# Optimization experiments

Measured on AMD Instinct MI355X. Metric: run time of the kernel, lower is better.

The kernel has to match this reference:

```python
import jax, jax.numpy as jnp
import numpy as np
from jax import lax

BN_EPS = 1e-3
SLOPE = 0.1
CLUSTER_TEMP = 30.0
K = 16
FEAT = 4096  # 8*8*64


def conv_bn_lrelu(x, w, b, g, beta, m, v):
    # Conv2d stride 2, padding 1 (NCHW / OIHW), then eval-mode BatchNorm, then LeakyReLU.
    y = lax.conv_general_dilated(x, w, window_strides=(2, 2), padding=((1, 1), (1, 1)),
                                 dimension_numbers=("NCHW", "OIHW", "NCHW"))
    y = y + b[None, :, None, None]
    scale = g / jnp.sqrt(v + BN_EPS)
    y = y * scale[None, :, None, None] + (beta - m * scale)[None, :, None, None]
    return jnp.where(y > 0, y, SLOPE * y)


def soft_kmeans(data, mu, num_iter, ct):
    # Row L2-normalize (equivalent to diag(1/||x||) @ data)
    data = data / jnp.linalg.norm(data, axis=1, keepdims=True)
    for _ in range(num_iter):
        dist = data @ mu.T                      # [N, K]
        r = jax.nn.softmax(ct * dist, axis=1)   # [N, K]
        mu = (r.T @ data) / r.sum(axis=0)[:, None]  # [K, F]
    dist = data @ mu.T
    r = jax.nn.softmax(ct * dist, axis=1)
    return mu, r, dist


def setup_inputs() -> dict:
    key = jax.random.key(0)
    ks = jax.random.split(key, 12)
    d = {}
    d["x"] = jax.random.normal(ks[0], (256, 3, 64, 64), dtype=jnp.float32)
    # conv1: 3 -> 128
    d["conv1_w"] = jax.random.normal(ks[1], (128, 3, 3, 3), dtype=jnp.float32) * 0.05
    d["conv1_b"] = jnp.zeros((128,), jnp.float32)
    d["bn1_g"] = jnp.ones((128,), jnp.float32)
    d["bn1_b"] = jnp.zeros((128,), jnp.float32)
    d["bn1_m"] = jax.random.normal(ks[2], (128,), dtype=jnp.float32) * 0.1
    d["bn1_v"] = jax.random.uniform(ks[3], (128,), minval=0.5, maxval=1.5, dtype=jnp.float32)
    # conv2: 128 -> 256
    d["conv2_w"] = jax.random.normal(ks[4], (256, 128, 3, 3), dtype=jnp.float32) * 0.02
    d["conv2_b"] = jnp.zeros((256,), jnp.float32)
    d["bn2_g"] = jnp.ones((256,), jnp.float32)
    d["bn2_b"] = jnp.zeros((256,), jnp.float32)
    d["bn2_m"] = jax.random.normal(ks[5], (256,), dtype=jnp.float32) * 0.1
    d["bn2_v"] = jax.random.uniform(ks[6], (256,), minval=0.5, maxval=1.5, dtype=jnp.float32)
    # conv3: 256 -> 64
    d["conv3_w"] = jax.random.normal(ks[7], (64, 256, 3, 3), dtype=jnp.float32) * 0.02
    d["conv3_b"] = jnp.zeros((64,), jnp.float32)
    d["bn3_g"] = jnp.ones((64,), jnp.float32)
    d["bn3_b"] = jnp.zeros((64,), jnp.float32)
    d["bn3_m"] = jax.random.normal(ks[8], (64,), dtype=jnp.float32) * 0.1
    d["bn3_v"] = jax.random.uniform(ks[9], (64,), minval=0.5, maxval=1.5, dtype=jnp.float32)
    # initial cluster centers, torch.rand(K, F)
    d["mu0"] = jax.random.uniform(ks[10], (K, FEAT), dtype=jnp.float32)
    d["num_iter"] = 10
    return d


def reference(x, conv1_w, conv1_b, bn1_g, bn1_b, bn1_m, bn1_v,
              conv2_w, conv2_b, bn2_g, bn2_b, bn2_m, bn2_v,
              conv3_w, conv3_b, bn3_g, bn3_b, bn3_m, bn3_v,
              mu0, num_iter):
    h = conv_bn_lrelu(x, conv1_w, conv1_b, bn1_g, bn1_b, bn1_m, bn1_v)   # [B,128,32,32]
    h = conv_bn_lrelu(h, conv2_w, conv2_b, bn2_g, bn2_b, bn2_m, bn2_v)   # [B,256,16,16]
    h = conv_bn_lrelu(h, conv3_w, conv3_b, bn3_g, bn3_b, bn3_m, bn3_v)   # [B,64,8,8]
    embeds = h.reshape(-1, FEAT)                                          # [B, 4096]
    mu_init, _, _ = soft_kmeans(embeds, mu0, num_iter, CLUSTER_TEMP)
    _, r, _ = soft_kmeans(embeds, lax.stop_gradient(mu_init), 1, CLUSTER_TEMP)
    return r
```

## Files before the change

kernel.cpp:

```cpp
#include <hip/hip_runtime.h>
#include <stdint.h>
#include <stddef.h>

typedef unsigned short u16;
typedef __attribute__((ext_vector_type(8))) short short8;
typedef __attribute__((ext_vector_type(4))) float f32x4;
typedef __attribute__((ext_vector_type(4))) int int4v;

__device__ __forceinline__ float bf2f(u16 u) {
    unsigned x = ((unsigned)u) << 16;
    return __uint_as_float(x);
}
__device__ __forceinline__ u16 f2bf(float f) {
    unsigned x = __float_as_uint(f);
    unsigned r = (x + 0x7fffu + ((x >> 16) & 1u)) >> 16;
    return (u16)r;
}
__device__ __forceinline__ float ldin(const void* p, size_t i, int isbf) {
    return isbf ? bf2f(((const u16*)p)[i]) : ((const float*)p)[i];
}
__device__ __forceinline__ int detect_bf(const void* v1) {
    const u16* ub = (const u16*)v1;
    int ok = 1;
#pragma unroll
    for (int i = 0; i < 16; i++) {
        float f = bf2f(ub[i]);
        if (!(f >= 0.4f && f <= 1.6f)) ok = 0;
    }
    return ok;
}
__device__ __forceinline__ int sw(int r, int c8) {
    return r * 32 + (((c8) ^ (r & 3)) << 3);
}

struct PrepArgs {
    const void *w1, *w2, *w3;
    u16 *W1p, *W2p, *W3p;
    const void *b1, *g1, *be1, *m1, *v1;
    const void *b2, *g2, *be2, *m2, *v2;
    const void *b3, *g3, *be3, *m3, *v3;
    float *es1, *esh1, *es2, *esh2, *es3, *esh3;
};
__device__ __forceinline__ void packw_body(const void* src, u16* dst, int CI, int Kp,
                                           int total, int blk, int t, int isbf) {
    int p = blk * 256 + t;
    if (p >= total) return;
    int co = p / Kp, k = p - co * Kp;
    int tap = k / CI, ci = k - tap * CI;
    u16 v = 0;
    if (tap < 9) {
        size_t si = (size_t)(co * CI + ci) * 9 + tap;
        v = isbf ? ((const u16*)src)[si] : f2bf(((const float*)src)[si]);
    }
    dst[p] = v;
}
__global__ __launch_bounds__(256) void kprep_all(PrepArgs A) {
    int b = blockIdx.x, t = threadIdx.x;
    int isbf = detect_bf(A.v1);
    if (b < 1152) {
        packw_body(A.w2, A.W2p, 128, 1152, 256 * 1152, b, t, isbf);
    } else if (b < 1728) {
        packw_body(A.w3, A.W3p, 256, 2304, 64 * 2304, b - 1152, t, isbf);
    } else if (b < 1744) {
        packw_body(A.w1, A.W1p, 3, 32, 128 * 32, b - 1728, t, isbf);
    } else {
        int u = (b - 1744) * 256 + t;
        const void *bb, *g, *be, *m, *v;
        float *es, *esh;
        int c;
        if (u < 128)      { c = u;       bb=A.b1; g=A.g1; be=A.be1; m=A.m1; v=A.v1; es=A.es1; esh=A.esh1; }
        else if (u < 384) { c = u - 128; bb=A.b2; g=A.g2; be=A.be2; m=A.m2; v=A.v2; es=A.es2; esh=A.esh2; }
        else if (u < 448) { c = u - 384; bb=A.b3; g=A.g3; be=A.be3; m=A.m3; v=A.v3; es=A.es3; esh=A.esh3; }
        else return;
        float sc = ldin(g, c, isbf) / sqrtf(ldin(v, c, isbf) + 1e-3f);
        float sh = (ldin(bb, c, isbf) - ldin(m, c, isbf)) * sc + ldin(be, c, isbf);
        es[c] = sc;
        esh[c] = sh;
    }
}

__global__ void kfallback(u16* __restrict__ out) {
    int i = blockIdx.x * 256 + threadIdx.x;
    if (i < 4096) out[i] = f2bf(0.0625f);
}

__global__ __launch_bounds__(256) void im2col1(const void* __restrict__ x,
                                               u16* __restrict__ A1,
                                               const void* __restrict__ v1ref) {
    int n = blockIdx.x, t = threadIdx.x;
    int isbf = detect_bf(v1ref);
    __shared__ u16 xs[3 * 64 * 64];
    if (isbf) {
        const u16* xp = (const u16*)x + (size_t)n * 12288;
#pragma unroll
        for (int i = t * 8; i < 12288; i += 2048)
            *(int4v*)&xs[i] = *(const int4v*)&xp[i];
    } else {
        const float* xp = (const float*)x + (size_t)n * 12288;
#pragma unroll
        for (int i = t * 4; i < 12288; i += 1024) {
            float4 v = *(const float4*)&xp[i];
            xs[i] = f2bf(v.x); xs[i + 1] = f2bf(v.y);
            xs[i + 2] = f2bf(v.z); xs[i + 3] = f2bf(v.w);
        }
    }
    __syncthreads();
#pragma unroll
    for (int rr = 0; rr < 4; rr++) {
        int m = rr * 256 + t;
        int ox = m & 31, oy = m >> 5;
        alignas(16) u16 row[32];
#pragma unroll
        for (int k = 0; k < 32; k++) {
            u16 val = 0;
            if (k < 27) {
                int tap = k / 3, ci = k - 3 * tap;
                int ky = tap / 3, kx = tap - 3 * ky;
                int iy = 2 * oy - 1 + ky, ix = 2 * ox - 1 + kx;
                if ((unsigned)iy < 64u && (unsigned)ix < 64u)
                    val = xs[ci * 4096 + iy * 64 + ix];
            }
            row[k] = val;
        }
        int4v* dst = (int4v*)(A1 + ((size_t)n * 1024 + m) * 32);
        const int4v* srcv = (const int4v*)row;
#pragma unroll
        for (int q = 0; q < 4; q++) dst[q] = srcv[q];
    }
}

__global__ __launch_bounds__(256) void gemm_conv1(
    const u16* __restrict__ A1, const u16* __restrict__ W,
    const float* __restrict__ es, const float* __restrict__ esh,
    u16* __restrict__ OutB) {
    alignas(16) __shared__ u16 As[128 * 32];
    alignas(16) __shared__ u16 Bs[128 * 32];
    const int t = threadIdx.x;
    const int m0 = blockIdx.x * 128;
    const int lane = t & 63, w = t >> 6;
    const int wm = w & 1, wn = w >> 1;
    const int rA = t >> 2, c8 = t & 3, koff = c8 * 8;

#pragma unroll
    for (int j = 0; j < 2; j++) {
        int4v va = *(const int4v*)(A1 + (size_t)(m0 + j * 64 + rA) * 32 + koff);
        *(int4v*)&As[sw(j * 64 + rA, c8)] = va;
        int4v vb = *(const int4v*)(W + (size_t)(j * 64 + rA) * 32 + koff);
        *(int4v*)&Bs[sw(j * 64 + rA, c8)] = vb;
    }
    __syncthreads();
    const int qc = lane >> 4, fr = lane & 15;
    short8 af[4], bf[4];
#pragma unroll
    for (int i = 0; i < 4; i++) af[i] = *(const short8*)&As[sw(wm * 64 + i * 16 + fr, qc)];
#pragma unroll
    for (int j = 0; j < 4; j++) bf[j] = *(const short8*)&Bs[sw(wn * 64 + j * 16 + fr, qc)];
    f32x4 acc[4][4];
#pragma unroll
    for (int i = 0; i < 4; i++)
#pragma unroll
        for (int j = 0; j < 4; j++) {
#pragma unroll
            for (int q = 0; q < 4; q++) acc[i][j][q] = 0.f;
            acc[i][j] = __builtin_amdgcn_mfma_f32_16x16x32_bf16(af[i], bf[j], acc[i][j], 0, 0, 0);
        }
#pragma unroll
    for (int j = 0; j < 4; j++) {
        int c = wn * 64 + j * 16 + fr;
        float sc = es[c], sh = esh[c];
#pragma unroll
        for (int i = 0; i < 4; i++) {
#pragma unroll
            for (int rg = 0; rg < 4; rg++) {
                int m = m0 + wm * 64 + i * 16 + qc * 4 + rg;
                float v = acc[i][j][rg] * sc + sh;
                v = (v > 0.f) ? v : 0.1f * v;
                int ox = m & 31, oy = (m >> 5) & 31, n = m >> 10;
                OutB[((size_t)(n * 32 + oy) * 32 + ox) * 128 + c] = f2bf(v);
            }
        }
    }
}

__global__ __launch_bounds__(256) void gemm_conv2(
    const u16* __restrict__ Asrc, const u16* __restrict__ W,
    const float* __restrict__ es, const float* __restrict__ esh,
    u16* __restrict__ OutB) {
    constexpr int CIN = 128, KTOT = 1152, OHW = 16, LOG_OHW = 4, IH = 32;
    constexpr int CC = 4, AR = 2, BR = 2, SM = 4, SN = 4;

    alignas(16) __shared__ u16 As[128 * 32];
    alignas(16) __shared__ u16 Bs[128 * 32];

    const int t = threadIdx.x;
    const int lid = blockIdx.x;
    const int xcd = lid & 7, slot = lid >> 3;
    const int img = xcd * 32 + (slot >> 2);
    const int sub = slot & 3;
    const int m0 = img * 256 + (sub & 1) * 128;
    const int n0 = (sub >> 1) * 128;
    const int lane = t & 63, w = t >> 6;
    const int wm = w & 1, wn = w >> 1;
    const int rA = t >> 2, c8 = t & 3, koff = c8 * 8;
    const int fr = lane & 15, qc = lane >> 4;

    f32x4 acc[SM][SN];
#pragma unroll
    for (int i = 0; i < SM; i++)
#pragma unroll
        for (int j = 0; j < SN; j++)
#pragma unroll
            for (int q = 0; q < 4; q++) acc[i][j][q] = 0.0f;

    int aox[AR], aoy[AR], an_[AR];
#pragma unroll
    for (int j = 0; j < AR; j++) {
        int m = m0 + j * 64 + rA;
        aox[j] = m & (OHW - 1);
        aoy[j] = (m >> LOG_OHW) & (OHW - 1);
        an_[j] = m >> (2 * LOG_OHW);
    }
    auto mkoffs = [&](int j, int tap) -> int {
        int ky = tap / 3, kx = tap - 3 * ky;
        int iy = 2 * aoy[j] - 1 + ky, ix = 2 * aox[j] - 1 + kx;
        if ((unsigned)iy < (unsigned)IH && (unsigned)ix < (unsigned)IH)
            return ((an_[j] * IH + iy) * IH + ix) * CIN;
        return -0x40000000;
    };
    const u16* Wrow[BR];
#pragma unroll
    for (int j = 0; j < BR; j++)
        Wrow[j] = W + (size_t)(n0 + j * 64 + rA) * KTOT + koff;

    int offs_cur[AR], offs_nxt[AR];
#pragma unroll
    for (int j = 0; j < AR; j++) offs_cur[j] = mkoffs(j, 0);

    const int4v zerov = (int4v){0, 0, 0, 0};
    int4v bufA[2][AR], bufB[2][BR];
#pragma unroll
    for (int pp = 0; pp < 2; pp++) {
#pragma unroll
        for (int j = 0; j < AR; j++)
            bufA[pp][j] = (offs_cur[j] >= 0)
                              ? *(const int4v*)(Asrc + offs_cur[j] + pp * 32 + koff)
                              : zerov;
#pragma unroll
        for (int j = 0; j < BR; j++) bufB[pp][j] = *(const int4v*)(Wrow[j] + pp * 32);
    }

    int flat = 0;
    for (int tap = 0; tap < 9; tap++) {
#pragma unroll
        for (int j = 0; j < AR; j++)
            offs_nxt[j] = (tap < 8) ? mkoffs(j, tap + 1) : -0x40000000;
#pragma unroll
        for (int cc = 0; cc < CC; cc++, flat++) {
            const int pb_ = flat & 1;
#pragma unroll
            for (int j = 0; j < AR; j++) *(int4v*)&As[sw(j * 64 + rA, c8)] = bufA[pb_][j];
#pragma unroll
            for (int j = 0; j < BR; j++) *(int4v*)&Bs[sw(j * 64 + rA, c8)] = bufB[pb_][j];
            __syncthreads();
            {
                const int cc2 = cc + 2;
                const bool intap = (cc2 < CC);
                const int cci = intap ? cc2 : cc2 - CC;
                const int aoffbase = cci * 32 + koff;
#pragma unroll
                for (int j = 0; j < AR; j++) {
                    int o = intap ? offs_cur[j] : offs_nxt[j];
                    bufA[pb_][j] = (o >= 0) ? *(const int4v*)(Asrc + o + aoffbase) : zerov;
                }
                const bool wvalid = intap || (tap < 8);
                const int wk = (intap ? tap : tap + 1) * CIN + cci * 32;
#pragma unroll
                for (int j = 0; j < BR; j++)
                    bufB[pb_][j] = wvalid ? *(const int4v*)(Wrow[j] + wk) : zerov;
            }
            short8 af[SM], bf[SN];
#pragma unroll
            for (int i = 0; i < SM; i++)
                af[i] = *(const short8*)&As[sw(wm * 64 + i * 16 + fr, qc)];
#pragma unroll
            for (int j = 0; j < SN; j++)
                bf[j] = *(const short8*)&Bs[sw(wn * 64 + j * 16 + fr, qc)];
#pragma unroll
            for (int i = 0; i < SM; i++)
#pragma unroll
                for (int j = 0; j < SN; j++)
                    acc[i][j] = __builtin_amdgcn_mfma_f32_16x16x32_bf16(
                        af[i], bf[j], acc[i][j], 0, 0, 0);
            __syncthreads();
        }
#pragma unroll
        for (int j = 0; j < AR; j++) offs_cur[j] = offs_nxt[j];
    }

#pragma unroll
    for (int j = 0; j < SN; j++) {
        int c = n0 + wn * 64 + j * 16 + fr;
        float sc = es[c], sh = esh[c];
#pragma unroll
        for (int i = 0; i < SM; i++) {
#pragma unroll
            for (int rg = 0; rg < 4; rg++) {
                int row = wm * 64 + i * 16 + qc * 4 + rg;
                int m = m0 + row;
                float v = acc[i][j][rg] * sc + sh;
                v = (v > 0.f) ? v : 0.1f * v;
                int ox = m & (OHW - 1), oy = (m >> LOG_OHW) & (OHW - 1), n = m >> (2 * LOG_OHW);
                OutB[((size_t)(n * 16 + oy) * 16 + ox) * 256 + c] = f2bf(v);
            }
        }
    }
}

__global__ __launch_bounds__(256) void gemm_conv3f(
    const u16* __restrict__ Asrc, const u16* __restrict__ W,
    const float* __restrict__ es3, const float* __restrict__ esh3,
    float* __restrict__ dat, u16* __restrict__ datbf) {
    constexpr int CIN = 256, KTOT = 2304, IH = 16;
    constexpr int CC = 8, SM = 2, SN = 2;

    alignas(16) __shared__ u16 As[64 * 32];
    alignas(16) __shared__ u16 Bs[64 * 32];
    __shared__ float red[4];

    const int t = threadIdx.x;
    const int lid = blockIdx.x;
    const int xcd = lid & 7, slot = lid >> 3;
    const int img = xcd * 32 + slot;
    const int m0 = img * 64;
    const int lane = t & 63, w = t >> 6;
    const int wm = w & 1, wn = w >> 1;
    const int rA = t >> 2, c8 = t & 3, koff = c8 * 8;
    const int fr = lane & 15, qc = lane >> 4;

    f32x4 acc[SM][SN];
#pragma unroll
    for (int i = 0; i < SM; i++)
#pragma unroll
        for (int j = 0; j < SN; j++)
#pragma unroll
            for (int q = 0; q < 4; q++) acc[i][j][q] = 0.0f;

    const int aox = rA & 7, aoy = (rA >> 3) & 7;
    auto mkoffs = [&](int tap) -> int {
        int ky = tap / 3, kx = tap - 3 * ky;
        int iy = 2 * aoy - 1 + ky, ix = 2 * aox - 1 + kx;
        if ((unsigned)iy < (unsigned)IH && (unsigned)ix < (unsigned)IH)
            return ((img * IH + iy) * IH + ix) * CIN;
        return -0x40000000;
    };
    const u16* Wrow = W + (size_t)rA * KTOT + koff;

    int offs_cur = mkoffs(0), offs_nxt;
    const int4v zerov = (int4v){0, 0, 0, 0};
    int4v bufA[2], bufB[2];
#pragma unroll
    for (int pp = 0; pp < 2; pp++) {
        bufA[pp] = (offs_cur >= 0)
                       ? *(const int4v*)(Asrc + offs_cur + pp * 32 + koff)
                       : zerov;
        bufB[pp] = *(const int4v*)(Wrow + pp * 32);
    }

    int flat = 0;
    for (int tap = 0; tap < 9; tap++) {
        offs_nxt = (tap < 8) ? mkoffs(tap + 1) : -0x40000000;
#pragma unroll
        for (int cc = 0; cc < CC; cc++, flat++) {
            const int pb_ = flat & 1;
            *(int4v*)&As[sw(rA, c8)] = bufA[pb_];
            *(int4v*)&Bs[sw(rA, c8)] = bufB[pb_];
            __syncthreads();
            {
                const int cc2 = cc + 2;
                const bool intap = (cc2 < CC);
                const int cci = intap ? cc2 : cc2 - CC;
                int o = intap ? offs_cur : offs_nxt;
                bufA[pb_] = (o >= 0) ? *(const int4v*)(Asrc + o + cci * 32 + koff) : zerov;
                const bool wvalid = intap || (tap < 8);
                const int wk = (intap ? tap : tap + 1) * CIN + cci * 32;
                bufB[pb_] = wvalid ? *(const int4v*)(Wrow + wk) : zerov;
            }
            short8 af[SM], bf[SN];
#pragma unroll
            for (int i = 0; i < SM; i++)
                af[i] = *(const short8*)&As[sw(wm * 32 + i * 16 + fr, qc)];
#pragma unroll
            for (int j = 0; j < SN; j++)
                bf[j] = *(const short8*)&Bs[sw(wn * 32 + j * 16 + fr, qc)];
#pragma unroll
            for (int i = 0; i < SM; i++)
#pragma unroll
                for (int j = 0; j < SN; j++)
                    acc[i][j] = __builtin_amdgcn_mfma_f32_16x16x32_bf16(
                        af[i], bf[j], acc[i][j], 0, 0, 0);
            __syncthreads();
        }
        offs_cur = offs_nxt;
    }

    float vals[SM][SN][4];
    float ssq = 0.f;
#pragma unroll
    for (int j = 0; j < SN; j++) {
        int c = wn * 32 + j * 16 + fr;
        float sc = es3[c], sh = esh3[c];
#pragma unroll
        for (int i = 0; i < SM; i++) {
#pragma unroll
            for (int rg = 0; rg < 4; rg++) {
                float v = acc[i][j][rg] * sc + sh;
                v = (v > 0.f) ? v : 0.1f * v;
                vals[i][j][rg] = v;
                ssq += v * v;
            }
        }
    }
#pragma unroll
    for (int off = 32; off > 0; off >>= 1) ssq += __shfl_xor(ssq, off);
    if (lane == 0) red[w] = ssq;
    __syncthreads();
    float inv = 1.0f / sqrtf(red[0] + red[1] + red[2] + red[3]);
#pragma unroll
    for (int j = 0; j < SN; j++) {
        int c = wn * 32 + j * 16 + fr;
#pragma unroll
        for (int i = 0; i < SM; i++) {
#pragma unroll
            for (int rg = 0; rg < 4; rg++) {
                int row = wm * 32 + i * 16 + qc * 4 + rg;
                size_t idx = (size_t)img * 4096 + c * 64 + row;
                float v = vals[i][j][rg] * inv;
                dat[idx] = v;
                datbf[idx] = f2bf(v);
            }
        }
    }
}

__global__ __launch_bounds__(256) void kgr(const u16* __restrict__ dbf,
                                           const float* __restrict__ dat,
                                           const void* __restrict__ mu0,
                                           u16* __restrict__ Ghi,
                                           u16* __restrict__ Glo,
                                           float* __restrict__ rb0,
                                           const void* __restrict__ v1ref) {
    const int b = blockIdx.x, t = threadIdx.x;
    alignas(16) __shared__ u16 As[64 * 32];
    alignas(16) __shared__ u16 Bs[64 * 32];
    __shared__ float part[16][4];
    __shared__ float ds[16];

    if (b < 16) {
        const int m0 = (b & 3) * 64, n0 = (b >> 2) * 64;
        const int lane = t & 63, w = t >> 6;
        const int wm = w & 1, wn = w >> 1;
        const int rA = t >> 2, c8 = t & 3, koff = c8 * 8;

        f32x4 acc[2][2];
#pragma unroll
        for (int i = 0; i < 2; i++)
#pragma unroll
            for (int j = 0; j < 2; j++)
#pragma unroll
                for (int q = 0; q < 4; q++) acc[i][j][q] = 0.0f;

        int4v pa = *(const int4v*)(dbf + (size_t)(m0 + rA) * 4096 + koff);
        int4v pb = *(const int4v*)(dbf + (size_t)(n0 + rA) * 4096 + koff);
        for (int it = 0; it < 128; it++) {
            *(int4v*)&As[sw(rA, c8)] = pa;
            *(int4v*)&Bs[sw(rA, c8)] = pb;
            __syncthreads();
            if (it + 1 < 128) {
                int k = (it + 1) * 32 + koff;
                pa = *(const int4v*)(dbf + (size_t)(m0 + rA) * 4096 + k);
                pb = *(const int4v*)(dbf + (size_t)(n0 + rA) * 4096 + k);
            }
            const int qc = lane >> 4, fr = lane & 15;
            short8 af[2], bf[2];
#pragma unroll
            for (int i = 0; i < 2; i++) af[i] = *(const short8*)&As[sw(wm * 32 + i * 16 + fr, qc)];
#pragma unroll
            for (int j = 0; j < 2; j++) bf[j] = *(const short8*)&Bs[sw(wn * 32 + j * 16 + fr, qc)];
#pragma unroll
            for (int i = 0; i < 2; i++)
#pragma unroll
                for (int j = 0; j < 2; j++)
                    acc[i][j] = __builtin_amdgcn_mfma_f32_16x16x32_bf16(af[i], bf[j], acc[i][j], 0, 0, 0);
            if (it + 1 < 128) __syncthreads();
        }
#pragma unroll
        for (int j = 0; j < 2; j++) {
            int c = n0 + wn * 32 + j * 16 + (lane & 15);
#pragma unroll
            for (int i = 0; i < 2; i++)
#pragma unroll
                for (int rg = 0; rg < 4; rg++) {
                    int row = m0 + wm * 32 + i * 16 + (lane >> 4) * 4 + rg;
                    float v = acc[i][j][rg];
                    u16 hi = f2bf(v);
                    u16 lo = f2bf(v - bf2f(hi));
                    Ghi[(size_t)row * 256 + c] = hi;
                    Glo[(size_t)row * 256 + c] = lo;
                }
        }
    } else {
        const int n = b - 16;
        const int isbf = detect_bf(v1ref);
        const int lane = t & 63, wv = t >> 6;
        float d[16];
#pragma unroll
        for (int j = 0; j < 16; j++) d[j] = dat[(size_t)n * 4096 + j * 256 + t];
#pragma unroll
        for (int k = 0; k < 16; k++) {
            float a = 0.f;
            if (isbf) {
                const u16* mp = (const u16*)mu0 + (size_t)k * 4096;
#pragma unroll
                for (int j = 0; j < 16; j++) a = fmaf(d[j], bf2f(mp[j * 256 + t]), a);
            } else {
                const float* mp = (const float*)mu0 + (size_t)k * 4096;
#pragma unroll
                for (int j = 0; j < 16; j++) a = fmaf(d[j], mp[j * 256 + t], a);
            }
#pragma unroll
            for (int off = 32; off > 0; off >>= 1) a += __shfl_xor(a, off);
            if (lane == 0) part[k][wv] = a;
        }
        __syncthreads();
        if (t < 16) {
            float dk = part[t][0] + part[t][1] + part[t][2] + part[t][3];
            ds[t] = dk;
            __syncthreads();
            float mx = -1e30f;
#pragma unroll
            for (int j = 0; j < 16; j++) mx = fmaxf(mx, ds[j]);
            float sum = 0.f;
#pragma unroll
            for (int j = 0; j < 16; j++) sum += __expf(30.f * (ds[j] - mx));
            rb0[n * 16 + t] = __expf(30.f * (dk - mx)) / sum;
        }
    }
}

__global__ __launch_bounds__(1024) void kmiter(const u16* __restrict__ Ghi,
                                               const u16* __restrict__ Glo,
                                               const float* __restrict__ rb0,
                                               void* __restrict__ dout,
                                               const void* __restrict__ v1ref) {
    const int t = threadIdx.x;
    const int isbf = detect_bf(v1ref);
    const int lane = t & 63, w = t >> 6;
    const int i0 = w * 16;
    const int col = lane & 15;
    const int q = lane >> 4;

    __shared__ float rf[4096];
    __shared__ u16 rThi[16 * 264];
    __shared__ u16 rTlo[16 * 264];
    __shared__ float part[16][17];
    __shared__ float rs[16];

    for (int idx = t; idx < 4096; idx += 1024) {
        float v = rb0[idx];
        rf[idx] = v;
        u16 hi = f2bf(v);
        rThi[(idx & 15) * 264 + (idx >> 4)] = hi;
        rTlo[(idx & 15) * 264 + (idx >> 4)] = f2bf(v - bf2f(hi));
    }
    __syncthreads();

    const u16* Ahirow = Ghi + (size_t)(i0 + col) * 256 + q * 8;
    const u16* Alorow = Glo + (size_t)(i0 + col) * 256 + q * 8;
    for (int iter = 0; iter < 11; iter++) {
        f32x4 acc = {0.f, 0.f, 0.f, 0.f};
#pragma unroll
        for (int ks = 0; ks < 256; ks += 32) {
            short8 ah = *(const short8*)(Ahirow + ks);
            short8 al = *(const short8*)(Alorow + ks);
            short8 bh = *(const short8*)&rThi[col * 264 + ks + q * 8];
            short8 bl = *(const short8*)&rTlo[col * 264 + ks + q * 8];
            acc = __builtin_amdgcn_mfma_f32_16x16x32_bf16(ah, bh, acc, 0, 0, 0);
            acc = __builtin_amdgcn_mfma_f32_16x16x32_bf16(al, bh, acc, 0, 0, 0);
            acc = __builtin_amdgcn_mfma_f32_16x16x32_bf16(ah, bl, acc, 0, 0, 0);
        }
        if (t < 256) {
            int kk = t & 15, g = t >> 4;
            float psum = 0.f;
#pragma unroll
            for (int nn = 0; nn < 16; nn++) psum += rf[(g * 16 + nn) * 16 + kk];
            part[kk][g] = psum;
        }
        __syncthreads();
        if (t < 16) {
            float ssum = 0.f;
#pragma unroll
            for (int g = 0; g < 16; g++) ssum += part[t][g];
            rs[t] = ssum;
        }
        __syncthreads();
        float rsc = rs[col];
        float rv[4];
#pragma unroll
        for (int rg = 0; rg < 4; rg++) {
            float dk = acc[rg] / rsc;
            float mx = dk;
#pragma unroll
            for (int o = 1; o < 16; o <<= 1) mx = fmaxf(mx, __shfl_xor(mx, o));
            float e = __expf(30.f * (dk - mx));
            float ssum = e;
#pragma unroll
            for (int o = 1; o < 16; o <<= 1) ssum += __shfl_xor(ssum, o);
            rv[rg] = e / ssum;
        }
        if (iter < 10) {
            __syncthreads();
#pragma unroll
            for (int rg = 0; rg < 4; rg++) {
                int row = i0 + q * 4 + rg;
                float v = rv[rg];
                rf[row * 16 + col] = v;
                u16 hi = f2bf(v);
                rThi[col * 264 + row] = hi;
                rTlo[col * 264 + row] = f2bf(v - bf2f(hi));
            }
            __syncthreads();
        } else {
#pragma unroll
            for (int rg = 0; rg < 4; rg++) {
                int row = i0 + q * 4 + rg;
                if (isbf) ((u16*)dout)[row * 16 + col] = f2bf(rv[rg]);
                else ((float*)dout)[row * 16 + col] = rv[rg];
            }
        }
    }
}

extern "C" void kernel_launch(void* const* d_in, const int* in_sizes, int n_in,
                              void* d_out, int out_size, void* d_ws, size_t ws_size,
                              hipStream_t stream) {
    const void* x   = d_in[0];
    const void* w1  = d_in[1];
    const void* b1  = d_in[2];
    const void* g1  = d_in[3];
    const void* be1 = d_in[4];
    const void* m1  = d_in[5];
    const void* v1  = d_in[6];
    const void* w2  = d_in[7];
    const void* b2  = d_in[8];
    const void* g2  = d_in[9];
    const void* be2 = d_in[10];
    const void* m2  = d_in[11];
    const void* v2  = d_in[12];
    const void* w3  = d_in[13];
    const void* b3  = d_in[14];
    const void* g3  = d_in[15];
    const void* be3 = d_in[16];
    const void* m3  = d_in[17];
    const void* v3  = d_in[18];
    const void* mu0 = d_in[19];

    char* p = (char*)d_ws;
    size_t used = 0;
    auto alloc = [&](size_t bytes) -> char* {
        char* q = p;
        size_t rb = (bytes + 255) & ~(size_t)255;
        p += rb;
        used += rb;
        return q;
    };
    float* rb0 = (float*)alloc(4096 * 4);
    u16* Ghi = (u16*)alloc((size_t)65536 * 2);
    u16* Glo = (u16*)alloc((size_t)65536 * 2);
    u16* W1p = (u16*)alloc((size_t)128 * 32 * 2);
    u16* W2p = (u16*)alloc((size_t)256 * 1152 * 2);
    u16* W3p = (u16*)alloc((size_t)64 * 2304 * 2);
    float* es1 = (float*)alloc(128 * 4);
    float* esh1 = (float*)alloc(128 * 4);
    float* es2 = (float*)alloc(256 * 4);
    float* esh2 = (float*)alloc(256 * 4);
    float* es3 = (float*)alloc(64 * 4);
    float* esh3 = (float*)alloc(64 * 4);
    const size_t R1 = (size_t)256 * 32 * 32 * 128 * 2;
    const size_t R2 = (size_t)256 * 16 * 16 * 256 * 2;
    char* reg1 = alloc(R1);
    char* reg2 = alloc(R2);
    u16* h1 = (u16*)reg1;
    u16* A1 = (u16*)reg2;
    u16* h2 = (u16*)reg2;
    float* dat = (float*)reg1;
    u16* datbf = (u16*)(reg1 + 4194304);

    if (used > ws_size) {
        kfallback<<<16, 256, 0, stream>>>((u16*)d_out);
        return;
    }

    PrepArgs pa = {w1, w2, w3, W1p, W2p, W3p,
                   b1, g1, be1, m1, v1, b2, g2, be2, m2, v2, b3, g3, be3, m3, v3,
                   es1, esh1, es2, esh2, es3, esh3};
    kprep_all<<<1746, 256, 0, stream>>>(pa);
    im2col1<<<256, 256, 0, stream>>>(x, A1, v1);
    gemm_conv1<<<dim3(2048), 256, 0, stream>>>(A1, W1p, es1, esh1, h1);
    gemm_conv2<<<dim3(1024), 256, 0, stream>>>(h1, W2p, es2, esh2, h2);
    gemm_conv3f<<<dim3(256), 256, 0, stream>>>(h2, W3p, es3, esh3, dat, datbf);
    kgr<<<dim3(272), 256, 0, stream>>>(datbf, dat, mu0, Ghi, Glo, rb0, v1);
    kmiter<<<1, 1024, 0, stream>>>(Ghi, Glo, rb0, d_out, v1);
}
```

Baseline: 291.7 us.

## Fuse conv1 im2col into GEMM and split conv3 K-loop across two warp groups

Conv1's separate im2col kernel is removed. Each GEMM block now loads a 9-row input slab into shared memory, builds its A tile there, and reads weights straight from global memory, so the im2col buffer no longer makes a round trip through HBM. Conv3 now runs 512 threads per block, and two 256-thread groups each take half of the 72 K-chunks. Their partial sums are reduced through shared memory before the BN, LeakyReLU and L2-normalise epilogue. This doubles the waves working on each of the 256 blocks, at the cost of extra LDS and one more synchronisation.

```diff
diff --git a/kernel.cpp b/kernel.cpp
--- a/kernel.cpp
+++ b/kernel.cpp
@@ -84,77 +84,69 @@
     if (i < 4096) out[i] = f2bf(0.0625f);
 }
 
-__global__ __launch_bounds__(256) void im2col1(const void* __restrict__ x,
-                                               u16* __restrict__ A1,
-                                               const void* __restrict__ v1ref) {
-    int n = blockIdx.x, t = threadIdx.x;
-    int isbf = detect_bf(v1ref);
-    __shared__ u16 xs[3 * 64 * 64];
-    if (isbf) {
-        const u16* xp = (const u16*)x + (size_t)n * 12288;
-#pragma unroll
-        for (int i = t * 8; i < 12288; i += 2048)
-            *(int4v*)&xs[i] = *(const int4v*)&xp[i];
-    } else {
-        const float* xp = (const float*)x + (size_t)n * 12288;
-#pragma unroll
-        for (int i = t * 4; i < 12288; i += 1024) {
-            float4 v = *(const float4*)&xp[i];
-            xs[i] = f2bf(v.x); xs[i + 1] = f2bf(v.y);
-            xs[i + 2] = f2bf(v.z); xs[i + 3] = f2bf(v.w);
-        }
-    }
+__global__ __launch_bounds__(256) void conv1f(
+    const void* __restrict__ x, const u16* __restrict__ W,
+    const float* __restrict__ es, const float* __restrict__ esh,
+    u16* __restrict__ OutB, const void* __restrict__ v1ref) {
+    alignas(16) __shared__ u16 xs[3 * 9 * 64 + 8];
+    alignas(16) __shared__ u16 As[128 * 32];
+    const int t = threadIdx.x;
+    const int isbf = detect_bf(v1ref);
+    const int lid = blockIdx.x;
+    const int xcd = lid & 7, slot = lid >> 3;
+    const int img = xcd * 32 + (slot >> 3);
+    const int sub = slot & 7;
+    const int oy0 = sub * 4;
+    const int iy0 = 2 * oy0 - 1;
+
+    for (int idx = t; idx < 1728; idx += 256) {
+        int ci = idx / 576;
+        int rem = idx - ci * 576;
+        int iyr = rem >> 6, ix = rem & 63;
+        int iy = iy0 + iyr;
+        u16 v = 0;
+        if ((unsigned)iy < 64u) {
+            size_t si = ((size_t)(img * 3 + ci) * 64 + iy) * 64 + ix;
+            v = isbf ? ((const u16*)x)[si] : f2bf(((const float*)x)[si]);
+        }
+        xs[idx] = v;
+    }
+    const int lane = t & 63, w = t >> 6;
+    const int wm = w & 1, wn = w >> 1;
+    const int fr = lane & 15, qc = lane >> 4, qk = qc * 8;
+    short8 bf[4];
+#pragma unroll
+    for (int j = 0; j < 4; j++)
+        bf[j] = *(const short8*)(W + (size_t)(wn * 64 + j * 16 + fr) * 32 + qk);
     __syncthreads();
-#pragma unroll
-    for (int rr = 0; rr < 4; rr++) {
-        int m = rr * 256 + t;
-        int ox = m & 31, oy = m >> 5;
-        alignas(16) u16 row[32];
-#pragma unroll
-        for (int k = 0; k < 32; k++) {
+
+    {
+        const int r = t >> 1, half = t & 1;
+        const int ox = r & 31;
+        const int dy = 2 * (r >> 5);
+        alignas(16) u16 rowk[16];
+#pragma unroll
+        for (int kk = 0; kk < 16; kk++) {
+            int k = half * 16 + kk;
             u16 val = 0;
             if (k < 27) {
                 int tap = k / 3, ci = k - 3 * tap;
                 int ky = tap / 3, kx = tap - 3 * ky;
-                int iy = 2 * oy - 1 + ky, ix = 2 * ox - 1 + kx;
-                if ((unsigned)iy < 64u && (unsigned)ix < 64u)
-                    val = xs[ci * 4096 + iy * 64 + ix];
-            }
-            row[k] = val;
-        }
-        int4v* dst = (int4v*)(A1 + ((size_t)n * 1024 + m) * 32);
-        const int4v* srcv = (const int4v*)row;
-#pragma unroll
-        for (int q = 0; q < 4; q++) dst[q] = srcv[q];
-    }
-}
-
-__global__ __launch_bounds__(256) void gemm_conv1(
-    const u16* __restrict__ A1, const u16* __restrict__ W,
-    const float* __restrict__ es, const float* __restrict__ esh,
-    u16* __restrict__ OutB) {
-    alignas(16) __shared__ u16 As[128 * 32];
-    alignas(16) __shared__ u16 Bs[128 * 32];
-    const int t = threadIdx.x;
-    const int m0 = blockIdx.x * 128;
-    const int lane = t & 63, w = t >> 6;
-    const int wm = w & 1, wn = w >> 1;
-    const int rA = t >> 2, c8 = t & 3, koff = c8 * 8;
-
-#pragma unroll
-    for (int j = 0; j < 2; j++) {
-        int4v va = *(const int4v*)(A1 + (size_t)(m0 + j * 64 + rA) * 32 + koff);
-        *(int4v*)&As[sw(j * 64 + rA, c8)] = va;
-        int4v vb = *(const int4v*)(W + (size_t)(j * 64 + rA) * 32 + koff);
-        *(int4v*)&Bs[sw(j * 64 + rA, c8)] = vb;
+                int iyr = dy + ky;
+                int ix = 2 * ox - 1 + kx;
+                if ((unsigned)ix < 64u)
+                    val = xs[ci * 576 + iyr * 64 + ix];
+            }
+            rowk[kk] = val;
+        }
+        *(int4v*)&As[sw(r, half * 2 + 0)] = ((const int4v*)rowk)[0];
+        *(int4v*)&As[sw(r, half * 2 + 1)] = ((const int4v*)rowk)[1];
     }
     __syncthreads();
-    const int qc = lane >> 4, fr = lane & 15;
-    short8 af[4], bf[4];
+
+    short8 af[4];
 #pragma unroll
     for (int i = 0; i < 4; i++) af[i] = *(const short8*)&As[sw(wm * 64 + i * 16 + fr, qc)];
-#pragma unroll
-    for (int j = 0; j < 4; j++) bf[j] = *(const short8*)&Bs[sw(wn * 64 + j * 16 + fr, qc)];
     f32x4 acc[4][4];
 #pragma unroll
     for (int i = 0; i < 4; i++)
@@ -172,11 +164,12 @@
         for (int i = 0; i < 4; i++) {
 #pragma unroll
             for (int rg = 0; rg < 4; rg++) {
-                int m = m0 + wm * 64 + i * 16 + qc * 4 + rg;
+                int lr = wm * 64 + i * 16 + qc * 4 + rg;
+                int lm = sub * 128 + lr;
+                int ox = lm & 31, oy = lm >> 5;
                 float v = acc[i][j][rg] * sc + sh;
                 v = (v > 0.f) ? v : 0.1f * v;
-                int ox = m & 31, oy = (m >> 5) & 31, n = m >> 10;
-                OutB[((size_t)(n * 32 + oy) * 32 + ox) * 128 + c] = f2bf(v);
+                OutB[((size_t)(img * 32 + oy) * 32 + ox) * 128 + c] = f2bf(v);
             }
         }
     }
@@ -316,127 +309,139 @@
     }
 }
 
-__global__ __launch_bounds__(256) void gemm_conv3f(
+__global__ __launch_bounds__(512) void gemm_conv3f(
     const u16* __restrict__ Asrc, const u16* __restrict__ W,
     const float* __restrict__ es3, const float* __restrict__ esh3,
     float* __restrict__ dat, u16* __restrict__ datbf) {
     constexpr int CIN = 256, KTOT = 2304, IH = 16;
-    constexpr int CC = 8, SM = 2, SN = 2;
-
-    alignas(16) __shared__ u16 As[64 * 32];
-    alignas(16) __shared__ u16 Bs[64 * 32];
-    __shared__ float red[4];
+
+    alignas(16) __shared__ u16 As[2][64 * 32];
+    alignas(16) __shared__ u16 Bs[2][64 * 32];
+    __shared__ float redacc[64 * 64];
+    __shared__ float red2[4];
 
     const int t = threadIdx.x;
+    const int g = t >> 8, tg = t & 255;
     const int lid = blockIdx.x;
     const int xcd = lid & 7, slot = lid >> 3;
     const int img = xcd * 32 + slot;
-    const int m0 = img * 64;
-    const int lane = t & 63, w = t >> 6;
+    const int lane = tg & 63, w = tg >> 6;
     const int wm = w & 1, wn = w >> 1;
-    const int rA = t >> 2, c8 = t & 3, koff = c8 * 8;
+    const int rA = tg >> 2, c8 = tg & 3, koff = c8 * 8;
     const int fr = lane & 15, qc = lane >> 4;
 
-    f32x4 acc[SM][SN];
-#pragma unroll
-    for (int i = 0; i < SM; i++)
-#pragma unroll
-        for (int j = 0; j < SN; j++)
+    f32x4 acc[2][2];
+#pragma unroll
+    for (int i = 0; i < 2; i++)
+#pragma unroll
+        for (int j = 0; j < 2; j++)
 #pragma unroll
             for (int q = 0; q < 4; q++) acc[i][j][q] = 0.0f;
 
     const int aox = rA & 7, aoy = (rA >> 3) & 7;
-    auto mkoffs = [&](int tap) -> int {
+    auto aoffs = [&](int chunk) -> int {
+        int tap = chunk >> 3, cc = chunk & 7;
         int ky = tap / 3, kx = tap - 3 * ky;
         int iy = 2 * aoy - 1 + ky, ix = 2 * aox - 1 + kx;
         if ((unsigned)iy < (unsigned)IH && (unsigned)ix < (unsigned)IH)
-            return ((img * IH + iy) * IH + ix) * CIN;
+            return ((img * IH + iy) * IH + ix) * CIN + cc * 32;
         return -0x40000000;
     };
+    auto bko = [&](int chunk) -> int {
+        int tap = chunk >> 3, cc = chunk & 7;
+        return tap * CIN + cc * 32;
+    };
     const u16* Wrow = W + (size_t)rA * KTOT + koff;
-
-    int offs_cur = mkoffs(0), offs_nxt;
+    const int c0 = g * 36;
+
     const int4v zerov = (int4v){0, 0, 0, 0};
     int4v bufA[2], bufB[2];
 #pragma unroll
     for (int pp = 0; pp < 2; pp++) {
-        bufA[pp] = (offs_cur >= 0)
-                       ? *(const int4v*)(Asrc + offs_cur + pp * 32 + koff)
-                       : zerov;
-        bufB[pp] = *(const int4v*)(Wrow + pp * 32);
-    }
-
-    int flat = 0;
-    for (int tap = 0; tap < 9; tap++) {
-        offs_nxt = (tap < 8) ? mkoffs(tap + 1) : -0x40000000;
-#pragma unroll
-        for (int cc = 0; cc < CC; cc++, flat++) {
-            const int pb_ = flat & 1;
-            *(int4v*)&As[sw(rA, c8)] = bufA[pb_];
-            *(int4v*)&Bs[sw(rA, c8)] = bufB[pb_];
-            __syncthreads();
-            {
-                const int cc2 = cc + 2;
-                const bool intap = (cc2 < CC);
-                const int cci = intap ? cc2 : cc2 - CC;
-                int o = intap ? offs_cur : offs_nxt;
-                bufA[pb_] = (o >= 0) ? *(const int4v*)(Asrc + o + cci * 32 + koff) : zerov;
-                const bool wvalid = intap || (tap < 8);
-                const int wk = (intap ? tap : tap + 1) * CIN + cci * 32;
-                bufB[pb_] = wvalid ? *(const int4v*)(Wrow + wk) : zerov;
-            }
-            short8 af[SM], bf[SN];
-#pragma unroll
-            for (int i = 0; i < SM; i++)
-                af[i] = *(const short8*)&As[sw(wm * 32 + i * 16 + fr, qc)];
-#pragma unroll
-            for (int j = 0; j < SN; j++)
-                bf[j] = *(const short8*)&Bs[sw(wn * 32 + j * 16 + fr, qc)];
-#pragma unroll
-            for (int i = 0; i < SM; i++)
-#pragma unroll
-                for (int j = 0; j < SN; j++)
-                    acc[i][j] = __builtin_amdgcn_mfma_f32_16x16x32_bf16(
-                        af[i], bf[j], acc[i][j], 0, 0, 0);
-            __syncthreads();
-        }
-        offs_cur = offs_nxt;
-    }
-
-    float vals[SM][SN][4];
+        int o = aoffs(c0 + pp);
+        bufA[pp] = (o >= 0) ? *(const int4v*)(Asrc + o + koff) : zerov;
+        bufB[pp] = *(const int4v*)(Wrow + bko(c0 + pp));
+    }
+    for (int cidx = 0; cidx < 36; cidx++) {
+        const int pb_ = cidx & 1;
+        *(int4v*)&As[g][sw(rA, c8)] = bufA[pb_];
+        *(int4v*)&Bs[g][sw(rA, c8)] = bufB[pb_];
+        __syncthreads();
+        if (cidx + 2 < 36) {
+            int ch = c0 + cidx + 2;
+            int o = aoffs(ch);
+            bufA[pb_] = (o >= 0) ? *(const int4v*)(Asrc + o + koff) : zerov;
+            bufB[pb_] = *(const int4v*)(Wrow + bko(ch));
+        }
+        short8 af[2], bf[2];
+#pragma unroll
+        for (int i = 0; i < 2; i++)
+            af[i] = *(const short8*)&As[g][sw(wm * 32 + i * 16 + fr, qc)];
+#pragma unroll
+        for (int j = 0; j < 2; j++)
+            bf[j] = *(const short8*)&Bs[g][sw(wn * 32 + j * 16 + fr, qc)];
+#pragma unroll
+        for (int i = 0; i < 2; i++)
+#pragma unroll
+            for (int j = 0; j < 2; j++)
+                acc[i][j] = __builtin_amdgcn_mfma_f32_16x16x32_bf16(
+                    af[i], bf[j], acc[i][j], 0, 0, 0);
+        __syncthreads();
+    }
+
+    if (g == 1) {
+#pragma unroll
+        for (int j = 0; j < 2; j++)
+#pragma unroll
+            for (int i = 0; i < 2; i++)
+#pragma unroll
+                for (int rg = 0; rg < 4; rg++) {
+                    int row = wm * 32 + i * 16 + qc * 4 + rg;
+                    int col = wn * 32 + j * 16 + fr;
+                    redacc[row * 64 + col] = acc[i][j][rg];
+                }
+    }
+    __syncthreads();
+    float vals[2][2][4];
     float ssq = 0.f;
-#pragma unroll
-    for (int j = 0; j < SN; j++) {
-        int c = wn * 32 + j * 16 + fr;
-        float sc = es3[c], sh = esh3[c];
-#pragma unroll
-        for (int i = 0; i < SM; i++) {
-#pragma unroll
-            for (int rg = 0; rg < 4; rg++) {
-                float v = acc[i][j][rg] * sc + sh;
-                v = (v > 0.f) ? v : 0.1f * v;
-                vals[i][j][rg] = v;
-                ssq += v * v;
-            }
-        }
-    }
-#pragma unroll
-    for (int off = 32; off > 0; off >>= 1) ssq += __shfl_xor(ssq, off);
-    if (lane == 0) red[w] = ssq;
+    if (g == 0) {
+#pragma unroll
+        for (int j = 0; j < 2; j++) {
+            int c = wn * 32 + j * 16 + fr;
+            float sc = es3[c], sh = esh3[c];
+#pragma unroll
+            for (int i = 0; i < 2; i++) {
+#pragma unroll
+                for (int rg = 0; rg < 4; rg++) {
+                    int row = wm * 32 + i * 16 + qc * 4 + rg;
+                    float v = acc[i][j][rg] + redacc[row * 64 + c];
+                    v = v * sc + sh;
+                    v = (v > 0.f) ? v : 0.1f * v;
+                    vals[i][j][rg] = v;
+                    ssq += v * v;
+                }
+            }
+        }
+#pragma unroll
+        for (int off = 32; off > 0; off >>= 1) ssq += __shfl_xor(ssq, off);
+        if (lane == 0) red2[w] = ssq;
+    }
     __syncthreads();
-    float inv = 1.0f / sqrtf(red[0] + red[1] + red[2] + red[3]);
-#pragma unroll
-    for (int j = 0; j < SN; j++) {
-        int c = wn * 32 + j * 16 + fr;
-#pragma unroll
-        for (int i = 0; i < SM; i++) {
-#pragma unroll
-            for (int rg = 0; rg < 4; rg++) {
-                int row = wm * 32 + i * 16 + qc * 4 + rg;
-                size_t idx = (size_t)img * 4096 + c * 64 + row;
-                float v = vals[i][j][rg] * inv;
-                dat[idx] = v;
-                datbf[idx] = f2bf(v);
+    if (g == 0) {
+        float inv = 1.0f / sqrtf(red2[0] + red2[1] + red2[2] + red2[3]);
+#pragma unroll
+        for (int j = 0; j < 2; j++) {
+            int c = wn * 32 + j * 16 + fr;
+#pragma unroll
+            for (int i = 0; i < 2; i++) {
+#pragma unroll
+                for (int rg = 0; rg < 4; rg++) {
+                    int row = wm * 32 + i * 16 + qc * 4 + rg;
+                    size_t idx = (size_t)img * 4096 + c * 64 + row;
+                    float v = vals[i][j][rg] * inv;
+                    dat[idx] = v;
+                    datbf[idx] = f2bf(v);
+                }
             }
         }
     }
@@ -690,7 +695,6 @@
     char* reg1 = alloc(R1);
     char* reg2 = alloc(R2);
     u16* h1 = (u16*)reg1;
-    u16* A1 = (u16*)reg2;
     u16* h2 = (u16*)reg2;
     float* dat = (float*)reg1;
     u16* datbf = (u16*)(reg1 + 4194304);
@@ -704,10 +708,9 @@
                    b1, g1, be1, m1, v1, b2, g2, be2, m2, v2, b3, g3, be3, m3, v3,
                    es1, esh1, es2, esh2, es3, esh3};
     kprep_all<<<1746, 256, 0, stream>>>(pa);
-    im2col1<<<256, 256, 0, stream>>>(x, A1, v1);
-    gemm_conv1<<<dim3(2048), 256, 0, stream>>>(A1, W1p, es1, esh1, h1);
+    conv1f<<<dim3(2048), 256, 0, stream>>>(x, W1p, es1, esh1, h1, v1);
     gemm_conv2<<<dim3(1024), 256, 0, stream>>>(h1, W2p, es2, esh2, h2);
-    gemm_conv3f<<<dim3(256), 256, 0, stream>>>(h2, W3p, es3, esh3, dat, datbf);
+    gemm_conv3f<<<dim3(256), 512, 0, stream>>>(h2, W3p, es3, esh3, dat, datbf);
     kgr<<<dim3(272), 256, 0, stream>>>(datbf, dat, mu0, Ghi, Glo, rb0, v1);
     kmiter<<<1, 1024, 0, stream>>>(Ghi, Glo, rb0, d_out, v1);
 }
```

New measurement: 311.7 us. 1.07x slower.
